# Kernel tuning notes

Hardware: AMD Instinct MI355X
Metric: run time of the kernel (lower is better)

The kernel has to match this reference:

```python
import jax, jax.numpy as jnp
import numpy as np

B, L, NC, REG_MAX = 32, 8400, 15, 16
EPS_IOU = 0.1  # RotatedIoULoss eps (clamp min)


def _cross2(a, b):
    return a[..., 0] * b[..., 1] - a[..., 1] * b[..., 0]


def _box2corners(box):
    # box [...,5] = (x, y, w, h, alpha) -> corners [...,4,2], consistent cyclic order
    x, y, w, h, a = (box[..., i] for i in range(5))
    xo = jnp.array([0.5, -0.5, -0.5, 0.5], box.dtype)
    yo = jnp.array([-0.5, -0.5, 0.5, 0.5], box.dtype)
    px = w[..., None] * xo  # [...,4]
    py = h[..., None] * yo
    c, s = jnp.cos(a)[..., None], jnp.sin(a)[..., None]
    rx = c * px - s * py + x[..., None]
    ry = s * px + c * py + y[..., None]
    return jnp.stack([rx, ry], axis=-1)


def _box_intersection(c1, c2):
    # segment-segment intersections between the 4 edges of each box -> [N,16,2], valid [N,16]
    p1 = c1[:, :, None, :]
    p2 = jnp.roll(c1, -1, axis=-2)[:, :, None, :]
    q1 = c2[:, None, :, :]
    q2 = jnp.roll(c2, -1, axis=-2)[:, None, :, :]
    d1, d2, r = p2 - p1, q2 - q1, q1 - p1
    den = _cross2(d1, d2)
    safe = jnp.where(jnp.abs(den) < 1e-12, jnp.ones_like(den), den)
    t = _cross2(r, d2) / safe
    u = _cross2(r, d1) / safe
    valid = (jnp.abs(den) > 1e-12) & (t > 0) & (t < 1) & (u > 0) & (u < 1)
    pts = p1 + t[..., None] * d1
    pts = jnp.where(valid[..., None], pts, jnp.zeros_like(pts))
    N = c1.shape[0]
    return pts.reshape(N, 16, 2), valid.reshape(N, 16)


def _points_in_box(pts, corners):
    # pts [N,4,2] inside rotated box given by corners [N,4,2] (projection test)
    a = corners[:, 0:1]
    ab = corners[:, 1:2] - a
    ad = corners[:, 3:4] - a
    ap = pts - a
    pab = jnp.sum(ap * ab, -1)
    pad = jnp.sum(ap * ad, -1)
    nab = jnp.sum(ab * ab, -1)
    nad = jnp.sum(ad * ad, -1)
    return (pab >= 0) & (pab <= nab) & (pad >= 0) & (pad <= nad)


def _sorted_poly_area(verts, mask):
    # sort candidate vertices CCW around the centroid of valid ones, shoelace area
    mf = mask.astype(verts.dtype)
    nv = jnp.maximum(mf.sum(-1, keepdims=True), 1.0)  # [N,1]
    mean = (verts * mf[..., None]).sum(-2, keepdims=True) / nv[..., None]
    rel = verts - mean
    ang = jnp.where(mask, jnp.arctan2(rel[..., 1], rel[..., 0]), 1e6)
    order = jnp.argsort(ang, axis=-1)
    sv = jnp.take_along_axis(verts, order[..., None], axis=-2)
    sm = jnp.take_along_axis(mask, order, axis=-1)
    sv = jnp.where(sm[..., None], sv, sv[..., :1, :])  # pad invalid with first vertex
    nxt = jnp.roll(sv, -1, axis=-2)
    return 0.5 * jnp.abs(jnp.sum(sv[..., 0] * nxt[..., 1] - nxt[..., 0] * sv[..., 1], axis=-1))


def diff_iou_rotated_2d(box1, box2):
    # box1, box2: [N,5] -> iou [N]
    c1, c2 = _box2corners(box1), _box2corners(box2)
    ipts, ivalid = _box_intersection(c1, c2)
    m1 = _points_in_box(c1, c2)
    m2 = _points_in_box(c2, c1)
    verts = jnp.concatenate([c1, c2, ipts], axis=-2)   # [N,24,2]
    mask = jnp.concatenate([m1, m2, ivalid], axis=-1)  # [N,24]
    inter = _sorted_poly_area(verts, mask)
    area1 = box1[..., 2] * box1[..., 3]
    area2 = box2[..., 2] * box2[..., 3]
    return inter / (area1 + area2 - inter + 1e-9)


def setup_inputs() -> dict:
    key = jax.random.key(0)
    ks = jax.random.split(key, 8)
    wh_off = jnp.array([0.0, 0.0, 0.2, 0.2], jnp.float32)
    pred_bboxes = jax.random.uniform(ks[0], (B, L, 4), jnp.float32) + wh_off
    target_bboxes = jax.random.uniform(ks[1], (B, L, 4), jnp.float32) + wh_off
    pred_angles = 0.5 * jax.random.normal(ks[2], (B, L, 1), jnp.float32)      # radians
    target_angles = 90.0 * jax.random.uniform(ks[3], (B, L, 1), jnp.float32)  # degrees
    pred_dist = jax.random.normal(ks[4], (B, L, (REG_MAX + 1) * 4), jnp.float32)
    target_scores = jax.random.uniform(ks[5], (B, L, NC), jnp.float32)
    fg_mask = jax.random.bernoulli(ks[6], 0.25, (B, L))
    tss = jnp.sum(target_scores.sum(-1) * fg_mask.astype(jnp.float32))[None]
    anchor_points = jax.random.uniform(ks[7], (L, 2), jnp.float32)
    return {"pred_dist": pred_dist, "pred_bboxes": pred_bboxes, "pred_angles": pred_angles,
            "anchor_points": anchor_points, "target_bboxes": target_bboxes,
            "target_angles": target_angles, "target_scores": target_scores,
            "target_scores_sum": tss, "fg_mask": fg_mask}


def reference(pred_dist, pred_bboxes, pred_angles, anchor_points, target_bboxes,
              target_angles, target_scores, target_scores_sum, fg_mask):
    mf = fg_mask.astype(pred_bboxes.dtype).reshape(-1)          # [B*L]
    num_pos = mf.sum()
    pi = jnp.asarray(np.pi, pred_bboxes.dtype)
    pred_R = jnp.concatenate([pred_bboxes, pred_angles], -1).reshape(-1, 5)
    tgt_R = jnp.concatenate([target_bboxes, target_angles / 180.0 * pi], -1).reshape(-1, 5)
    ious = jnp.maximum(diff_iou_rotated_2d(pred_R, tgt_R), EPS_IOU)  # clamp(min=eps)
    bbox_weight = target_scores.sum(-1).reshape(-1)             # [B*L]
    loss_elem = (1.0 - ious) * bbox_weight * mf                 # masked per-anchor loss
    lsum = loss_elem.sum()
    lmean = lsum / jnp.maximum(num_pos, 1.0)
    loss_iou = jnp.where(target_scores_sum[0] == 0, lsum, lmean)
    loss_iou = jnp.where(num_pos > 0, loss_iou, 0.0)
    loss_dfl = pred_dist.sum() * 0.0
    return (loss_iou, loss_dfl)
```

## Files before the change

kernel.cpp:

```cpp
#include <hip/hip_runtime.h>
#include <math.h>

#define NCLS 15
#define NV 24


__global__ void zero_ws_kernel(float* ws) {
    if (threadIdx.x == 0) { ws[0] = 0.0f; ((int*)ws)[1] = 0; }
}

__global__ __launch_bounds__(256) void compact_kernel(
    const int* __restrict__ fg_mask, int n,
    int* __restrict__ cnt, int* __restrict__ idxbuf)
{
    const int i = blockIdx.x * 256 + threadIdx.x;
    const bool pos = (i < n) && (fg_mask[i] != 0);
    const unsigned long long b = __ballot(pos);
    const int lane = threadIdx.x & 63;
    const int wid  = threadIdx.x >> 6;
    const int prefix = __popcll(b & ((1ULL << lane) - 1ULL));
    const int wtotal = __popcll(b);

    __shared__ int wbase[4];
    if (lane == 0) wbase[wid] = wtotal;
    __syncthreads();
    if (threadIdx.x == 0) {
        const int t0 = wbase[0], t1 = wbase[1], t2 = wbase[2], t3 = wbase[3];
        const int base = atomicAdd(cnt, t0 + t1 + t2 + t3);
        wbase[0] = base;
        wbase[1] = base + t0;
        wbase[2] = base + t0 + t1;
        wbase[3] = base + t0 + t1 + t2;
    }
    __syncthreads();
    if (pos) idxbuf[wbase[wid] + prefix] = i;
}

#define CSWAP(A, B)                                                       \
    {                                                                     \
        const float ka = ang[A], kb = ang[B];                             \
        const bool sw = kb < ka;                                          \
        ang[A] = sw ? kb : ka; ang[B] = sw ? ka : kb;                     \
        const float xa = vx[A], xb = vx[B];                               \
        vx[A] = sw ? xb : xa; vx[B] = sw ? xa : xb;                       \
        const float ya = vy[A], yb = vy[B];                               \
        vy[A] = sw ? yb : ya; vy[B] = sw ? ya : yb;                       \
    }

__global__ __launch_bounds__(256) void rbox_iou_kernel(
    const float* __restrict__ pred_bboxes,
    const float* __restrict__ pred_angles,
    const float* __restrict__ target_bboxes,
    const float* __restrict__ target_angles,
    const float* __restrict__ target_scores,
    const int*   __restrict__ cnt,
    const int*   __restrict__ idxbuf,
    float* __restrict__ ws)
{
    const int count = *cnt;
    if ((int)(blockIdx.x * 256) >= count) return;

    const int j = blockIdx.x * 256 + threadIdx.x;
    float loss = 0.0f;

    if (j < count) {
        const int i = idxbuf[j];

        const float4 pb = reinterpret_cast<const float4*>(pred_bboxes)[i];
        const float4 tb = reinterpret_cast<const float4*>(target_bboxes)[i];
        const float pa = pred_angles[i];
        const float ta = (target_angles[i] / 180.0f) * (float)M_PI;

        float c1x[4], c1y[4], c2x[4], c2y[4];
        {
            const float xo[4] = { 0.5f, -0.5f, -0.5f, 0.5f };
            const float yo[4] = { -0.5f, -0.5f, 0.5f, 0.5f };
            float cs = cosf(pa), sn = sinf(pa);
#pragma unroll
            for (int k = 0; k < 4; ++k) {
                const float px = pb.z * xo[k], py = pb.w * yo[k];
                c1x[k] = cs * px - sn * py + pb.x;
                c1y[k] = sn * px + cs * py + pb.y;
            }
            cs = cosf(ta); sn = sinf(ta);
#pragma unroll
            for (int k = 0; k < 4; ++k) {
                const float px = tb.z * xo[k], py = tb.w * yo[k];
                c2x[k] = cs * px - sn * py + tb.x;
                c2y[k] = sn * px + cs * py + tb.y;
            }
        }

        float vx[NV], vy[NV];
        bool  vm[NV];

        {
            const float ax = c2x[0], ay = c2y[0];
            const float abx = c2x[1] - ax, aby = c2y[1] - ay;
            const float adx = c2x[3] - ax, ady = c2y[3] - ay;
            const float nab = abx * abx + aby * aby;
            const float nad = adx * adx + ady * ady;
#pragma unroll
            for (int k = 0; k < 4; ++k) {
                const float apx = c1x[k] - ax, apy = c1y[k] - ay;
                const float pab = apx * abx + apy * aby;
                const float pad = apx * adx + apy * ady;
                vx[k] = c1x[k]; vy[k] = c1y[k];
                vm[k] = (pab >= 0.0f) && (pab <= nab) && (pad >= 0.0f) && (pad <= nad);
            }
        }
        {
            const float ax = c1x[0], ay = c1y[0];
            const float abx = c1x[1] - ax, aby = c1y[1] - ay;
            const float adx = c1x[3] - ax, ady = c1y[3] - ay;
            const float nab = abx * abx + aby * aby;
            const float nad = adx * adx + ady * ady;
#pragma unroll
            for (int k = 0; k < 4; ++k) {
                const float apx = c2x[k] - ax, apy = c2y[k] - ay;
                const float pab = apx * abx + apy * aby;
                const float pad = apx * adx + apy * ady;
                vx[4 + k] = c2x[k]; vy[4 + k] = c2y[k];
                vm[4 + k] = (pab >= 0.0f) && (pab <= nab) && (pad >= 0.0f) && (pad <= nad);
            }
        }
#pragma unroll
        for (int a = 0; a < 4; ++a) {
            const float p1x = c1x[a], p1y = c1y[a];
            const float d1x = c1x[(a + 1) & 3] - p1x;
            const float d1y = c1y[(a + 1) & 3] - p1y;
#pragma unroll
            for (int b = 0; b < 4; ++b) {
                const float q1x = c2x[b], q1y = c2y[b];
                const float d2x = c2x[(b + 1) & 3] - q1x;
                const float d2y = c2y[(b + 1) & 3] - q1y;
                const float rx = q1x - p1x, ry = q1y - p1y;
                const float den = d1x * d2y - d1y * d2x;
                const float safe = (fabsf(den) < 1e-12f) ? 1.0f : den;
                const float t = (rx * d2y - ry * d2x) / safe;
                const float u = (rx * d1y - ry * d1x) / safe;
                const bool val = (fabsf(den) > 1e-12f) &&
                                 (t > 0.0f) && (t < 1.0f) &&
                                 (u > 0.0f) && (u < 1.0f);
                const int idx = 8 + a * 4 + b;
                vx[idx] = val ? (p1x + t * d1x) : 0.0f;
                vy[idx] = val ? (p1y + t * d1y) : 0.0f;
                vm[idx] = val;
            }
        }

        float sx = 0.0f, sy = 0.0f, nvf = 0.0f;
#pragma unroll
        for (int k = 0; k < NV; ++k) {
            sx  += vm[k] ? vx[k] : 0.0f;
            sy  += vm[k] ? vy[k] : 0.0f;
            nvf += vm[k] ? 1.0f : 0.0f;
        }
        const float nv = fmaxf(nvf, 1.0f);
        const float mx = sx / nv, my = sy / nv;

        float ang[NV];
#pragma unroll
        for (int k = 0; k < NV; ++k) {
            const float rx = vx[k] - mx, ry = vy[k] - my;
            const float d = fabsf(rx) + fabsf(ry);
            const float a = rx / d;
            float p = (ry >= 0.0f) ? (1.0f - a) : (3.0f + a);
            if (d == 0.0f) p = 0.0f;
            ang[k] = vm[k] ? p : INFINITY;
        }

#pragma unroll
        for (int p = 1; p < 32; p <<= 1) {
#pragma unroll
            for (int k = p; k >= 1; k >>= 1) {
#pragma unroll
                for (int jj = k & (p - 1); jj + k < 32; jj += 2 * k) {
#pragma unroll
                    for (int ii = 0; ii < k; ++ii) {
                        if (ii + jj + k < 32 &&
                            ((ii + jj) / (2 * p)) == ((ii + jj + k) / (2 * p))) {
                            if (ii + jj + k < NV) {
                                CSWAP(ii + jj, ii + jj + k);
                            }
                        }
                    }
                }
            }
        }

        const float v0x = vx[0], v0y = vy[0];
        float total = 0.0f;
#pragma unroll
        for (int k = 0; k < NV; ++k) {
            const bool vk = ang[k] < INFINITY;
            const bool vn = (k < NV - 1) ? (ang[k + 1] < INFINITY) : false;
            const float nx = vn ? vx[k + 1] : v0x;
            const float ny = vn ? vy[k + 1] : v0y;
            total += vk ? (vx[k] * ny - nx * vy[k]) : 0.0f;
        }
        const float inter = 0.5f * fabsf(total);

        const float area1 = pb.z * pb.w;
        const float area2 = tb.z * tb.w;
        float iou = inter / (area1 + area2 - inter + 1e-9f);
        iou = fmaxf(iou, 0.1f);

        float w = 0.0f;
        const float* sp = target_scores + (size_t)i * NCLS;
#pragma unroll
        for (int k = 0; k < NCLS; ++k) w += sp[k];

        loss = (1.0f - iou) * w;
    }

#pragma unroll
    for (int off = 32; off > 0; off >>= 1)
        loss += __shfl_down(loss, off, 64);
    __shared__ float sl[4];
    const int lane = threadIdx.x & 63;
    const int wid  = threadIdx.x >> 6;
    if (lane == 0) sl[wid] = loss;
    __syncthreads();
    if (threadIdx.x == 0)
        atomicAdd(&ws[0], sl[0] + sl[1] + sl[2] + sl[3]);
}

__global__ void finalize_kernel(const float* __restrict__ ws,
                                const float* __restrict__ tss,
                                float* __restrict__ out)
{
    const float lsum = ws[0];
    const float npos = (float)((const int*)ws)[1];
    const float lmean = lsum / fmaxf(npos, 1.0f);
    float li = (tss[0] == 0.0f) ? lsum : lmean;
    li = (npos > 0.0f) ? li : 0.0f;
    out[0] = li;
    out[1] = 0.0f;
}

extern "C" void kernel_launch(void* const* d_in, const int* in_sizes, int n_in,
                              void* d_out, int out_size, void* d_ws, size_t ws_size,
                              hipStream_t stream) {
    const float* pred_bboxes   = (const float*)d_in[1];
    const float* pred_angles   = (const float*)d_in[2];
    const float* target_bboxes = (const float*)d_in[4];
    const float* target_angles = (const float*)d_in[5];
    const float* target_scores = (const float*)d_in[6];
    const float* tss           = (const float*)d_in[7];
    const int*   fg_mask       = (const int*)d_in[8];

    float* ws     = (float*)d_ws;
    int*   cnt    = (int*)d_ws + 1;
    int*   idxbuf = (int*)d_ws + 16;
    float* out    = (float*)d_out;

    const int n = in_sizes[8];
    const int blocks = (n + 255) / 256;

    zero_ws_kernel<<<1, 64, 0, stream>>>(ws);
    compact_kernel<<<blocks, 256, 0, stream>>>(fg_mask, n, cnt, idxbuf);
    rbox_iou_kernel<<<blocks, 256, 0, stream>>>(
        pred_bboxes, pred_angles, target_bboxes, target_angles,
        target_scores, cnt, idxbuf, ws);
    finalize_kernel<<<1, 1, 0, stream>>>(ws, tss, out);
}
```

Before: 152.3 us.

## Fuse compaction, IoU loss and finalize into one kernel with block-local compaction

```diff
diff --git a/kernel.cpp b/kernel.cpp
--- a/kernel.cpp
+++ b/kernel.cpp
@@ -3,38 +3,8 @@
 
 #define NCLS 15
 #define NV 24
-
-
-__global__ void zero_ws_kernel(float* ws) {
-    if (threadIdx.x == 0) { ws[0] = 0.0f; ((int*)ws)[1] = 0; }
-}
-
-__global__ __launch_bounds__(256) void compact_kernel(
-    const int* __restrict__ fg_mask, int n,
-    int* __restrict__ cnt, int* __restrict__ idxbuf)
-{
-    const int i = blockIdx.x * 256 + threadIdx.x;
-    const bool pos = (i < n) && (fg_mask[i] != 0);
-    const unsigned long long b = __ballot(pos);
-    const int lane = threadIdx.x & 63;
-    const int wid  = threadIdx.x >> 6;
-    const int prefix = __popcll(b & ((1ULL << lane) - 1ULL));
-    const int wtotal = __popcll(b);
-
-    __shared__ int wbase[4];
-    if (lane == 0) wbase[wid] = wtotal;
-    __syncthreads();
-    if (threadIdx.x == 0) {
-        const int t0 = wbase[0], t1 = wbase[1], t2 = wbase[2], t3 = wbase[3];
-        const int base = atomicAdd(cnt, t0 + t1 + t2 + t3);
-        wbase[0] = base;
-        wbase[1] = base + t0;
-        wbase[2] = base + t0 + t1;
-        wbase[3] = base + t0 + t1 + t2;
-    }
-    __syncthreads();
-    if (pos) idxbuf[wbase[wid] + prefix] = i;
-}
+#define EPB 1024
+
 
 #define CSWAP(A, B)                                                       \
     {                                                                     \
@@ -47,196 +17,224 @@
         vy[A] = sw ? yb : ya; vy[B] = sw ? ya : yb;                       \
     }
 
-__global__ __launch_bounds__(256) void rbox_iou_kernel(
+__device__ __forceinline__ float elem_loss(
+    int i,
+    const float* __restrict__ pred_bboxes,
+    const float* __restrict__ pred_angles,
+    const float* __restrict__ target_bboxes,
+    const float* __restrict__ target_angles,
+    const float* __restrict__ target_scores)
+{
+    const float4 pb = reinterpret_cast<const float4*>(pred_bboxes)[i];
+    const float4 tb = reinterpret_cast<const float4*>(target_bboxes)[i];
+    const float pa = pred_angles[i];
+    const float ta = (target_angles[i] / 180.0f) * (float)M_PI;
+
+    float c1x[4], c1y[4], c2x[4], c2y[4];
+    {
+        const float xo[4] = { 0.5f, -0.5f, -0.5f, 0.5f };
+        const float yo[4] = { -0.5f, -0.5f, 0.5f, 0.5f };
+        float cs = cosf(pa), sn = sinf(pa);
+#pragma unroll
+        for (int k = 0; k < 4; ++k) {
+            const float px = pb.z * xo[k], py = pb.w * yo[k];
+            c1x[k] = cs * px - sn * py + pb.x;
+            c1y[k] = sn * px + cs * py + pb.y;
+        }
+        cs = cosf(ta); sn = sinf(ta);
+#pragma unroll
+        for (int k = 0; k < 4; ++k) {
+            const float px = tb.z * xo[k], py = tb.w * yo[k];
+            c2x[k] = cs * px - sn * py + tb.x;
+            c2y[k] = sn * px + cs * py + tb.y;
+        }
+    }
+
+    float vx[NV], vy[NV];
+    bool  vm[NV];
+
+    {
+        const float ax = c2x[0], ay = c2y[0];
+        const float abx = c2x[1] - ax, aby = c2y[1] - ay;
+        const float adx = c2x[3] - ax, ady = c2y[3] - ay;
+        const float nab = abx * abx + aby * aby;
+        const float nad = adx * adx + ady * ady;
+#pragma unroll
+        for (int k = 0; k < 4; ++k) {
+            const float apx = c1x[k] - ax, apy = c1y[k] - ay;
+            const float pab = apx * abx + apy * aby;
+            const float pad = apx * adx + apy * ady;
+            vx[k] = c1x[k]; vy[k] = c1y[k];
+            vm[k] = (pab >= 0.0f) && (pab <= nab) && (pad >= 0.0f) && (pad <= nad);
+        }
+    }
+    {
+        const float ax = c1x[0], ay = c1y[0];
+        const float abx = c1x[1] - ax, aby = c1y[1] - ay;
+        const float adx = c1x[3] - ax, ady = c1y[3] - ay;
+        const float nab = abx * abx + aby * aby;
+        const float nad = adx * adx + ady * ady;
+#pragma unroll
+        for (int k = 0; k < 4; ++k) {
+            const float apx = c2x[k] - ax, apy = c2y[k] - ay;
+            const float pab = apx * abx + apy * aby;
+            const float pad = apx * adx + apy * ady;
+            vx[4 + k] = c2x[k]; vy[4 + k] = c2y[k];
+            vm[4 + k] = (pab >= 0.0f) && (pab <= nab) && (pad >= 0.0f) && (pad <= nad);
+        }
+    }
+#pragma unroll
+    for (int a = 0; a < 4; ++a) {
+        const float p1x = c1x[a], p1y = c1y[a];
+        const float d1x = c1x[(a + 1) & 3] - p1x;
+        const float d1y = c1y[(a + 1) & 3] - p1y;
+#pragma unroll
+        for (int b = 0; b < 4; ++b) {
+            const float q1x = c2x[b], q1y = c2y[b];
+            const float d2x = c2x[(b + 1) & 3] - q1x;
+            const float d2y = c2y[(b + 1) & 3] - q1y;
+            const float rx = q1x - p1x, ry = q1y - p1y;
+            const float den = d1x * d2y - d1y * d2x;
+            const float safe = (fabsf(den) < 1e-12f) ? 1.0f : den;
+            const float t = (rx * d2y - ry * d2x) / safe;
+            const float u = (rx * d1y - ry * d1x) / safe;
+            const bool val = (fabsf(den) > 1e-12f) &&
+                             (t > 0.0f) && (t < 1.0f) &&
+                             (u > 0.0f) && (u < 1.0f);
+            const int idx = 8 + a * 4 + b;
+            vx[idx] = val ? (p1x + t * d1x) : 0.0f;
+            vy[idx] = val ? (p1y + t * d1y) : 0.0f;
+            vm[idx] = val;
+        }
+    }
+
+    float sx = 0.0f, sy = 0.0f, nvf = 0.0f;
+#pragma unroll
+    for (int k = 0; k < NV; ++k) {
+        sx  += vm[k] ? vx[k] : 0.0f;
+        sy  += vm[k] ? vy[k] : 0.0f;
+        nvf += vm[k] ? 1.0f : 0.0f;
+    }
+    const float nv = fmaxf(nvf, 1.0f);
+    const float mx = sx / nv, my = sy / nv;
+
+    float ang[NV];
+#pragma unroll
+    for (int k = 0; k < NV; ++k) {
+        const float rx = vx[k] - mx, ry = vy[k] - my;
+        const float d = fabsf(rx) + fabsf(ry);
+        const float a = rx / d;
+        float p = (ry >= 0.0f) ? (1.0f - a) : (3.0f + a);
+        if (d == 0.0f) p = 0.0f;
+        ang[k] = vm[k] ? p : INFINITY;
+    }
+
+#pragma unroll
+    for (int p = 1; p < 32; p <<= 1) {
+#pragma unroll
+        for (int k = p; k >= 1; k >>= 1) {
+#pragma unroll
+            for (int jj = k & (p - 1); jj + k < 32; jj += 2 * k) {
+#pragma unroll
+                for (int ii = 0; ii < k; ++ii) {
+                    if (ii + jj + k < 32 &&
+                        ((ii + jj) / (2 * p)) == ((ii + jj + k) / (2 * p))) {
+                        if (ii + jj + k < NV) {
+                            CSWAP(ii + jj, ii + jj + k);
+                        }
+                    }
+                }
+            }
+        }
+    }
+
+    const float v0x = vx[0], v0y = vy[0];
+    float total = 0.0f;
+#pragma unroll
+    for (int k = 0; k < NV; ++k) {
+        const bool vk = ang[k] < INFINITY;
+        const bool vn = (k < NV - 1) ? (ang[k + 1] < INFINITY) : false;
+        const float nx = vn ? vx[k + 1] : v0x;
+        const float ny = vn ? vy[k + 1] : v0y;
+        total += vk ? (vx[k] * ny - nx * vy[k]) : 0.0f;
+    }
+    const float inter = 0.5f * fabsf(total);
+
+    const float area1 = pb.z * pb.w;
+    const float area2 = tb.z * tb.w;
+    float iou = inter / (area1 + area2 - inter + 1e-9f);
+    iou = fmaxf(iou, 0.1f);
+
+    float w = 0.0f;
+    const float* sp = target_scores + (size_t)i * NCLS;
+#pragma unroll
+    for (int k = 0; k < NCLS; ++k) w += sp[k];
+
+    return (1.0f - iou) * w;
+}
+
+__global__ __launch_bounds__(256) void fused_loss_kernel(
     const float* __restrict__ pred_bboxes,
     const float* __restrict__ pred_angles,
     const float* __restrict__ target_bboxes,
     const float* __restrict__ target_angles,
     const float* __restrict__ target_scores,
-    const int*   __restrict__ cnt,
-    const int*   __restrict__ idxbuf,
-    float* __restrict__ ws)
+    const int*   __restrict__ fg_mask,
+    const float* __restrict__ tss,
+    float* __restrict__ ws,
+    float* __restrict__ out,
+    int n, int nblocks)
 {
-    const int count = *cnt;
-    if ((int)(blockIdx.x * 256) >= count) return;
-
-    const int j = blockIdx.x * 256 + threadIdx.x;
+    __shared__ int sidx[EPB];
+    __shared__ int scnt;
+    __shared__ float sl[4];
+    __shared__ bool slast;
+
+    const int tid = threadIdx.x;
+    if (tid == 0) scnt = 0;
+    __syncthreads();
+
+    const int base = blockIdx.x * EPB + tid * 4;
+    if (base < n) {
+        const int4 m = *reinterpret_cast<const int4*>(fg_mask + base);
+        if (m.x) sidx[atomicAdd(&scnt, 1)] = base + 0;
+        if (m.y) sidx[atomicAdd(&scnt, 1)] = base + 1;
+        if (m.z) sidx[atomicAdd(&scnt, 1)] = base + 2;
+        if (m.w) sidx[atomicAdd(&scnt, 1)] = base + 3;
+    }
+    __syncthreads();
+    const int lcnt = scnt;
+
     float loss = 0.0f;
-
-    if (j < count) {
-        const int i = idxbuf[j];
-
-        const float4 pb = reinterpret_cast<const float4*>(pred_bboxes)[i];
-        const float4 tb = reinterpret_cast<const float4*>(target_bboxes)[i];
-        const float pa = pred_angles[i];
-        const float ta = (target_angles[i] / 180.0f) * (float)M_PI;
-
-        float c1x[4], c1y[4], c2x[4], c2y[4];
-        {
-            const float xo[4] = { 0.5f, -0.5f, -0.5f, 0.5f };
-            const float yo[4] = { -0.5f, -0.5f, 0.5f, 0.5f };
-            float cs = cosf(pa), sn = sinf(pa);
-#pragma unroll
-            for (int k = 0; k < 4; ++k) {
-                const float px = pb.z * xo[k], py = pb.w * yo[k];
-                c1x[k] = cs * px - sn * py + pb.x;
-                c1y[k] = sn * px + cs * py + pb.y;
-            }
-            cs = cosf(ta); sn = sinf(ta);
-#pragma unroll
-            for (int k = 0; k < 4; ++k) {
-                const float px = tb.z * xo[k], py = tb.w * yo[k];
-                c2x[k] = cs * px - sn * py + tb.x;
-                c2y[k] = sn * px + cs * py + tb.y;
-            }
-        }
-
-        float vx[NV], vy[NV];
-        bool  vm[NV];
-
-        {
-            const float ax = c2x[0], ay = c2y[0];
-            const float abx = c2x[1] - ax, aby = c2y[1] - ay;
-            const float adx = c2x[3] - ax, ady = c2y[3] - ay;
-            const float nab = abx * abx + aby * aby;
-            const float nad = adx * adx + ady * ady;
-#pragma unroll
-            for (int k = 0; k < 4; ++k) {
-                const float apx = c1x[k] - ax, apy = c1y[k] - ay;
-                const float pab = apx * abx + apy * aby;
-                const float pad = apx * adx + apy * ady;
-                vx[k] = c1x[k]; vy[k] = c1y[k];
-                vm[k] = (pab >= 0.0f) && (pab <= nab) && (pad >= 0.0f) && (pad <= nad);
-            }
-        }
-        {
-            const float ax = c1x[0], ay = c1y[0];
-            const float abx = c1x[1] - ax, aby = c1y[1] - ay;
-            const float adx = c1x[3] - ax, ady = c1y[3] - ay;
-            const float nab = abx * abx + aby * aby;
-            const float nad = adx * adx + ady * ady;
-#pragma unroll
-            for (int k = 0; k < 4; ++k) {
-                const float apx = c2x[k] - ax, apy = c2y[k] - ay;
-                const float pab = apx * abx + apy * aby;
-                const float pad = apx * adx + apy * ady;
-                vx[4 + k] = c2x[k]; vy[4 + k] = c2y[k];
-                vm[4 + k] = (pab >= 0.0f) && (pab <= nab) && (pad >= 0.0f) && (pad <= nad);
-            }
-        }
-#pragma unroll
-        for (int a = 0; a < 4; ++a) {
-            const float p1x = c1x[a], p1y = c1y[a];
-            const float d1x = c1x[(a + 1) & 3] - p1x;
-            const float d1y = c1y[(a + 1) & 3] - p1y;
-#pragma unroll
-            for (int b = 0; b < 4; ++b) {
-                const float q1x = c2x[b], q1y = c2y[b];
-                const float d2x = c2x[(b + 1) & 3] - q1x;
-                const float d2y = c2y[(b + 1) & 3] - q1y;
-                const float rx = q1x - p1x, ry = q1y - p1y;
-                const float den = d1x * d2y - d1y * d2x;
-                const float safe = (fabsf(den) < 1e-12f) ? 1.0f : den;
-                const float t = (rx * d2y - ry * d2x) / safe;
-                const float u = (rx * d1y - ry * d1x) / safe;
-                const bool val = (fabsf(den) > 1e-12f) &&
-                                 (t > 0.0f) && (t < 1.0f) &&
-                                 (u > 0.0f) && (u < 1.0f);
-                const int idx = 8 + a * 4 + b;
-                vx[idx] = val ? (p1x + t * d1x) : 0.0f;
-                vy[idx] = val ? (p1y + t * d1y) : 0.0f;
-                vm[idx] = val;
-            }
-        }
-
-        float sx = 0.0f, sy = 0.0f, nvf = 0.0f;
-#pragma unroll
-        for (int k = 0; k < NV; ++k) {
-            sx  += vm[k] ? vx[k] : 0.0f;
-            sy  += vm[k] ? vy[k] : 0.0f;
-            nvf += vm[k] ? 1.0f : 0.0f;
-        }
-        const float nv = fmaxf(nvf, 1.0f);
-        const float mx = sx / nv, my = sy / nv;
-
-        float ang[NV];
-#pragma unroll
-        for (int k = 0; k < NV; ++k) {
-            const float rx = vx[k] - mx, ry = vy[k] - my;
-            const float d = fabsf(rx) + fabsf(ry);
-            const float a = rx / d;
-            float p = (ry >= 0.0f) ? (1.0f - a) : (3.0f + a);
-            if (d == 0.0f) p = 0.0f;
-            ang[k] = vm[k] ? p : INFINITY;
-        }
-
-#pragma unroll
-        for (int p = 1; p < 32; p <<= 1) {
-#pragma unroll
-            for (int k = p; k >= 1; k >>= 1) {
-#pragma unroll
-                for (int jj = k & (p - 1); jj + k < 32; jj += 2 * k) {
-#pragma unroll
-                    for (int ii = 0; ii < k; ++ii) {
-                        if (ii + jj + k < 32 &&
-                            ((ii + jj) / (2 * p)) == ((ii + jj + k) / (2 * p))) {
-                            if (ii + jj + k < NV) {
-                                CSWAP(ii + jj, ii + jj + k);
-                            }
-                        }
-                    }
-                }
-            }
-        }
-
-        const float v0x = vx[0], v0y = vy[0];
-        float total = 0.0f;
-#pragma unroll
-        for (int k = 0; k < NV; ++k) {
-            const bool vk = ang[k] < INFINITY;
-            const bool vn = (k < NV - 1) ? (ang[k + 1] < INFINITY) : false;
-            const float nx = vn ? vx[k + 1] : v0x;
-            const float ny = vn ? vy[k + 1] : v0y;
-            total += vk ? (vx[k] * ny - nx * vy[k]) : 0.0f;
-        }
-        const float inter = 0.5f * fabsf(total);
-
-        const float area1 = pb.z * pb.w;
-        const float area2 = tb.z * tb.w;
-        float iou = inter / (area1 + area2 - inter + 1e-9f);
-        iou = fmaxf(iou, 0.1f);
-
-        float w = 0.0f;
-        const float* sp = target_scores + (size_t)i * NCLS;
-#pragma unroll
-        for (int k = 0; k < NCLS; ++k) w += sp[k];
-
-        loss = (1.0f - iou) * w;
-    }
+    for (int k = tid; k < lcnt; k += 256)
+        loss += elem_loss(sidx[k], pred_bboxes, pred_angles,
+                          target_bboxes, target_angles, target_scores);
 
 #pragma unroll
     for (int off = 32; off > 0; off >>= 1)
         loss += __shfl_down(loss, off, 64);
-    __shared__ float sl[4];
-    const int lane = threadIdx.x & 63;
-    const int wid  = threadIdx.x >> 6;
+    const int lane = tid & 63;
+    const int wid  = tid >> 6;
     if (lane == 0) sl[wid] = loss;
     __syncthreads();
-    if (threadIdx.x == 0)
+    if (tid == 0) {
         atomicAdd(&ws[0], sl[0] + sl[1] + sl[2] + sl[3]);
-}
-
-__global__ void finalize_kernel(const float* __restrict__ ws,
-                                const float* __restrict__ tss,
-                                float* __restrict__ out)
-{
-    const float lsum = ws[0];
-    const float npos = (float)((const int*)ws)[1];
-    const float lmean = lsum / fmaxf(npos, 1.0f);
-    float li = (tss[0] == 0.0f) ? lsum : lmean;
-    li = (npos > 0.0f) ? li : 0.0f;
-    out[0] = li;
-    out[1] = 0.0f;
+        atomicAdd((int*)ws + 1, lcnt);
+        __threadfence();
+        const int done = atomicAdd((int*)ws + 2, 1);
+        slast = (done == nblocks - 1);
+    }
+    __syncthreads();
+
+    if (slast && tid == 0) {
+        const float lsum = atomicAdd(&ws[0], 0.0f);
+        const float npos = (float)atomicAdd((int*)ws + 1, 0);
+        const float lmean = lsum / fmaxf(npos, 1.0f);
+        float li = (tss[0] == 0.0f) ? lsum : lmean;
+        li = (npos > 0.0f) ? li : 0.0f;
+        out[0] = li;
+        out[1] = 0.0f;
+    }
 }
 
 extern "C" void kernel_launch(void* const* d_in, const int* in_sizes, int n_in,
@@ -250,18 +248,14 @@
     const float* tss           = (const float*)d_in[7];
     const int*   fg_mask       = (const int*)d_in[8];
 
-    float* ws     = (float*)d_ws;
-    int*   cnt    = (int*)d_ws + 1;
-    int*   idxbuf = (int*)d_ws + 16;
-    float* out    = (float*)d_out;
+    float* ws  = (float*)d_ws;
+    float* out = (float*)d_out;
 
     const int n = in_sizes[8];
-    const int blocks = (n + 255) / 256;
-
-    zero_ws_kernel<<<1, 64, 0, stream>>>(ws);
-    compact_kernel<<<blocks, 256, 0, stream>>>(fg_mask, n, cnt, idxbuf);
-    rbox_iou_kernel<<<blocks, 256, 0, stream>>>(
+    const int blocks = (n + EPB - 1) / EPB;
+
+    hipMemsetAsync(d_ws, 0, 16, stream);
+    fused_loss_kernel<<<blocks, 256, 0, stream>>>(
         pred_bboxes, pred_angles, target_bboxes, target_angles,
-        target_scores, cnt, idxbuf, ws);
-    finalize_kernel<<<1, 1, 0, stream>>>(ws, tss, out);
+        target_scores, fg_mask, tss, ws, out, n, blocks);
 }
```

After: 145.7 us. 4.4% less time.
